# Performance work log

Measured on AMD Instinct MI355X. Metric: run time of the kernel, lower is better.

The kernel has to match this reference:

```python
import jax, jax.numpy as jnp
import numpy as np

B, S, O = 65536, 32, 16  # batch, state_dim, observation_dim


def setup_inputs() -> dict:
    key = jax.random.key(0)
    k1, k2, k3, k4 = jax.random.split(key, 4)
    observation = jax.random.normal(k1, (B, O), dtype=jnp.float32)
    # SPD observation noise covariance per batch element
    L = 0.1 * jax.random.normal(k2, (B, O, O), dtype=jnp.float32)
    observation_noise = jnp.einsum('bij,bkj->bik', L, L) + 1e-3 * jnp.eye(O, dtype=jnp.float32)
    observation_matrix = 0.001 * jax.random.normal(k3, (O, S), dtype=jnp.float32)
    observation_bias = 1e-6 * jax.random.normal(k4, (O,), dtype=jnp.float32)
    prior_mean = jnp.zeros((S,), dtype=jnp.float32)
    prior_precision = jnp.eye(S, dtype=jnp.float32)
    return {
        'observation': observation,
        'observation_noise': observation_noise,
        'observation_matrix': observation_matrix,
        'observation_bias': observation_bias,
        'prior_mean': prior_mean,
        'prior_precision': prior_precision,
    }


def reference(observation, observation_noise, observation_matrix, observation_bias,
              prior_mean, prior_precision):
    # observation: [B, O]; observation_noise: [B, O, O]
    noise_prec = jnp.linalg.inv(observation_noise)                      # [B, O, O]
    HtR = jnp.einsum('os,bop->bsp', observation_matrix, noise_prec)     # H^T R^{-1}: [B, S, O]
    innovation_cov = jnp.einsum('bso,ot->bst', HtR, observation_matrix) # [B, S, S]
    posterior_covariance = jnp.linalg.inv(prior_precision + innovation_cov)  # [B, S, S]
    residual = jnp.einsum('bso,bo->bs', HtR, observation - observation_bias)[..., None]  # [B, S, 1]
    prior_term = (prior_precision @ prior_mean)[:, None]                # [S, 1]
    posterior_mean = posterior_covariance @ (prior_term + residual)     # [B, S, 1]
    return posterior_mean, posterior_covariance
```

## Files before the change

### kernel.cpp

```cpp
#include <hip/hip_runtime.h>
#include <hip/hip_bf16.h>


typedef __attribute__((ext_vector_type(8))) short bf16x8;
typedef __attribute__((ext_vector_type(4))) float f32x4;

__device__ __forceinline__ unsigned bf16rne(float f) {
    unsigned x = __float_as_uint(f);
    return (x + 0x7FFFu + ((x >> 16) & 1u)) >> 16;
}
__device__ __forceinline__ unsigned pack2(float a, float b) {
    return bf16rne(a) | (bf16rne(b) << 16);
}

__global__ void lgs_setup(const float* __restrict__ H, const float* __restrict__ bias,
                          const float* __restrict__ mu0, const float* __restrict__ P,
                          float* __restrict__ ws)
{
    __shared__ float pinv[32][33];
    __shared__ float Gsh[16][33];
    const int l = threadIdx.x;

    float m[32];
#pragma unroll
    for (int i = 0; i < 32; ++i)
        m[i] = (l < 32) ? P[i * 32 + l] : ((i == (l - 32)) ? 1.0f : 0.0f);

#pragma unroll
    for (int k = 0; k < 32; ++k) {
        float bc[32];
#pragma unroll
        for (int i = 0; i < 32; ++i) bc[i] = __shfl(m[i], k, 64);
        float a = m[k] * (1.0f / bc[k]);
#pragma unroll
        for (int i = 0; i < 32; ++i)
            if (i != k) m[i] -= bc[i] * a;
        m[k] = a;
    }
    if (l >= 32) {
        const int c = l - 32;
#pragma unroll
        for (int i = 0; i < 32; ++i) pinv[c][i] = m[i];
    }
    asm volatile("" ::: "memory");

    for (int idx = l; idx < 512; idx += 64) {
        int o = idx >> 5, s = idx & 31;
        float acc = 0.f;
        for (int u = 0; u < 32; ++u) acc += H[o * 32 + u] * pinv[s][u];
        Gsh[o][s] = acc;
    }
    asm volatile("" ::: "memory");

    for (int idx = l; idx < 256; idx += 64) {
        int j = idx >> 4, i = idx & 15;
        float acc = 0.f;
        for (int s = 0; s < 32; ++s) acc += Gsh[i][s] * H[j * 32 + s];
        ws[idx] = acc;
    }
    unsigned* wsu = (unsigned*)ws;
    for (int idx = l; idx < 512; idx += 64) {
        int r = idx >> 8, rem = idx & 255;
        int ll = rem >> 2, j = rem & 3;
        int mm = 16 * r + (ll & 15);
        int kb = (((ll >> 4) * 8) + 2 * j) & 15;
        wsu[768 + idx] = pack2(-0.5f * Gsh[kb][mm], -0.5f * Gsh[kb + 1][mm]);
    }
    for (int idx = l; idx < 1024; idx += 64) {
        int tt = idx >> 8, rem = idx & 255;
        int ll = rem >> 2, j = rem & 3;
        int row = 16 * (tt >> 1) + ((ll >> 4) << 2) + j;
        int col = 16 * (tt & 1) + (ll & 15);
        ws[1280 + idx] = pinv[col][row];
    }
    for (int idx = l; idx < 512; idx += 64) {
        int c = idx >> 8, rem = idx & 255;
        int ll = rem >> 2, j2 = rem & 3;
        int col = 16 * c + (ll & 15);
        int k = (((ll >> 4) * 8) + 2 * j2) & 15;
        wsu[2304 + idx] = pack2(0.5f * Gsh[k][col], 0.5f * Gsh[k + 1][col]);
    }
    if (l < 16) {
        float acc = bias[l];
        for (int s = 0; s < 32; ++s) acc += H[l * 32 + s] * mu0[s];
        ws[2816 + l] = acc;
    }
    if (l < 32) ws[2832 + l] = mu0[l];
}

#define BCAST16(x, K) __int_as_float(__builtin_amdgcn_ds_swizzle(__float_as_int(x), (((K) << 5) | 0x10)))

template <int K>
__device__ __forceinline__ void gj16(int t, float (&m)[16], float (&v)[16])
{
    if (t == K) m[K] = 1.0f / m[K];
    float bc[16];
#pragma unroll
    for (int i = 0; i < 16; ++i) bc[i] = BCAST16(m[i], K);
    float pk = m[K] * bc[K];
#pragma unroll
    for (int i = 0; i < 16; ++i)
        if (i != K) m[i] -= bc[i] * pk;
    m[K] = pk;
    float a = v[K] * bc[K];
#pragma unroll
    for (int i = 0; i < 16; ++i)
        if (i != K) v[i] -= bc[i] * a;
    v[K] = a;
}

__global__ __launch_bounds__(512, 4) void lgs_main(
    const float* __restrict__ obs, const float* __restrict__ noise,
    const float* __restrict__ ws,
    float* __restrict__ out_mean, float* __restrict__ out_cov, int B)
{
    __shared__ float ld[8192];

    const int tid  = threadIdx.x;
    const int l    = tid & 63;
    const int t    = tid & 15;
    const int slot = tid >> 4;
    const int wv   = tid >> 6;
    const int b    = blockIdx.x * 32 + slot;
    const int bb   = (b < B) ? b : (B - 1);

    const float* __restrict__ Acm  = ws;
    const float* __restrict__ cvec = ws + 2816;
    const float* __restrict__ m0v  = ws + 2832;

    float m[16], v[16];

    const float4* Rr = (const float4*)(noise + (size_t)bb * 256 + t * 16);
    const float4* Ar = (const float4*)(Acm + t * 16);
#pragma unroll
    for (int i = 0; i < 4; ++i) {
        float4 r = Rr[i], a = Ar[i];
        m[4*i+0] = r.x + a.x; m[4*i+1] = r.y + a.y;
        m[4*i+2] = r.z + a.z; m[4*i+3] = r.w + a.w;
    }
#pragma unroll
    for (int i = 0; i < 16; ++i) v[i] = (i == t) ? 1.0f : 0.0f;

    gj16<0>(t, m, v);   gj16<1>(t, m, v);   gj16<2>(t, m, v);   gj16<3>(t, m, v);
    gj16<4>(t, m, v);   gj16<5>(t, m, v);   gj16<6>(t, m, v);   gj16<7>(t, m, v);
    gj16<8>(t, m, v);   gj16<9>(t, m, v);   gj16<10>(t, m, v);  gj16<11>(t, m, v);
    gj16<12>(t, m, v);  gj16<13>(t, m, v);  gj16<14>(t, m, v);  gj16<15>(t, m, v);

    {
        const int xw = t & 3;
        float* wb = &ld[slot * 256 + t * 16];
        *(float4*)&wb[(0 ^ xw) << 2] = make_float4(v[0],  v[1],  v[2],  v[3]);
        *(float4*)&wb[(1 ^ xw) << 2] = make_float4(v[4],  v[5],  v[6],  v[7]);
        *(float4*)&wb[(2 ^ xw) << 2] = make_float4(v[8],  v[9],  v[10], v[11]);
        *(float4*)&wb[(3 ^ xw) << 2] = make_float4(v[12], v[13], v[14], v[15]);
    }

    const uint4*  AF4 = (const uint4*)(ws + 768);
    const uint4*  BG4 = (const uint4*)(ws + 2304);
    const float4* PF4 = (const float4*)(ws + 1280);
    uint4 a0u = AF4[l], a1u = AF4[64 + l];
    uint4 g0u = BG4[l], g1u = BG4[64 + l];
    bf16x8 A0, A1, Bg0, Bg1;
    __builtin_memcpy(&A0,  &a0u, 16);
    __builtin_memcpy(&A1,  &a1u, 16);
    __builtin_memcpy(&Bg0, &g0u, 16);
    __builtin_memcpy(&Bg1, &g1u, 16);
    float4 pq;
    f32x4 pfr0, pfr1, pfr2, pfr3;
    pq = PF4[l];        pfr0[0]=pq.x; pfr0[1]=pq.y; pfr0[2]=pq.z; pfr0[3]=pq.w;
    pq = PF4[64 + l];   pfr1[0]=pq.x; pfr1[1]=pq.y; pfr1[2]=pq.z; pfr1[3]=pq.w;
    pq = PF4[128 + l];  pfr2[0]=pq.x; pfr2[1]=pq.y; pfr2[2]=pq.z; pfr2[3]=pq.w;
    pq = PF4[192 + l];  pfr3[0]=pq.x; pfr3[1]=pq.y; pfr3[2]=pq.z; pfr3[3]=pq.w;

    const int ch = l & 15;
    const int gp = l >> 4;
    const int gq = (gp & 1) * 2;
    const int xq = ch & 3;
    const int xt = (ch & 1) << 2;
    const float4 cv = ((const float4*)cvec)[gp];
    const float mu0a = m0v[ch], mu0b = m0v[16 + ch];
    const f32x4 zero = {0.f, 0.f, 0.f, 0.f};

#pragma unroll
    for (int h = 0; h < 4; ++h) {
        const int sh  = wv * 4 + h;
        const int bh  = blockIdx.x * 32 + sh;
        const int bhc = (bh < B) ? bh : (B - 1);

        const float* qb = &ld[sh * 256 + ch * 16];
        float4 qa = *(const float4*)&qb[((gq    ) ^ xq) << 2];
        float4 qc = *(const float4*)&qb[((gq + 1) ^ xq) << 2];
        unsigned qarr[4] = { pack2(qa.x, qa.y), pack2(qa.z, qa.w),
                             pack2(qc.x, qc.y), pack2(qc.z, qc.w) };
        bf16x8 Qa; __builtin_memcpy(&Qa, qarr, 16);
        f32x4 d0 = __builtin_amdgcn_mfma_f32_16x16x32_bf16(Qa, Bg0, zero, 0, 0, 0);
        f32x4 d1 = __builtin_amdgcn_mfma_f32_16x16x32_bf16(Qa, Bg1, zero, 0, 0, 0);

        float4 yv = *(const float4*)(obs + (size_t)bhc * 16 + gp * 4);
        float z0 = yv.x - cv.x, z1 = yv.y - cv.y, z2 = yv.z - cv.z, z3 = yv.w - cv.w;
        float p0 = d0[0]*z0 + d0[1]*z1 + d0[2]*z2 + d0[3]*z3;
        float p1 = d1[0]*z0 + d1[1]*z1 + d1[2]*z2 + d1[3]*z3;
        p0 += __int_as_float(__builtin_amdgcn_ds_swizzle(__float_as_int(p0), 0x401F));
        p1 += __int_as_float(__builtin_amdgcn_ds_swizzle(__float_as_int(p1), 0x401F));
        p0 += __shfl_xor(p0, 32, 64);
        p1 += __shfl_xor(p1, 32, 64);
        if (bh < B) {
            if (gp == 0) out_mean[(size_t)bh * 32 + ch]      = mu0a + p0;
            if (gp == 1) out_mean[(size_t)bh * 32 + 16 + ch] = mu0b + p1;
        }

        unsigned* tb = (unsigned*)&ld[sh * 256];
        const int g2 = gp * 2;
        *(uint2*)&tb[      ch * 8 + (g2 ^ xt)] =
            make_uint2(pack2(d0[0], d0[1]), pack2(d0[2], d0[3]));
        *(uint2*)&tb[128 + ch * 8 + (g2 ^ xt)] =
            make_uint2(pack2(d1[0], d1[1]), pack2(d1[2], d1[3]));

        const int kp = (gp & 1) * 4;
        uint4 bu0 = *(const uint4*)&tb[      ch * 8 + (kp ^ xt)];
        uint4 bu1 = *(const uint4*)&tb[128 + ch * 8 + (kp ^ xt)];
        bf16x8 Bf0, Bf1;
        __builtin_memcpy(&Bf0, &bu0, 16);
        __builtin_memcpy(&Bf1, &bu1, 16);
        f32x4 s00 = __builtin_amdgcn_mfma_f32_16x16x32_bf16(A0, Bf0, pfr0, 0, 0, 0);
        f32x4 s01 = __builtin_amdgcn_mfma_f32_16x16x32_bf16(A0, Bf1, pfr1, 0, 0, 0);
        f32x4 s10 = __builtin_amdgcn_mfma_f32_16x16x32_bf16(A1, Bf0, pfr2, 0, 0, 0);
        f32x4 s11 = __builtin_amdgcn_mfma_f32_16x16x32_bf16(A1, Bf1, pfr3, 0, 0, 0);

        if (bh < B) {
            float* Sb = out_cov + (size_t)bh * 1024 + (gp * 4) * 32 + ch;
#pragma unroll
            for (int j = 0; j < 4; ++j) {
                Sb[j * 32]       = s00[j];
                Sb[j * 32 + 16]  = s01[j];
                Sb[j * 32 + 512] = s10[j];
                Sb[j * 32 + 528] = s11[j];
            }
        }
    }
}

extern "C" void kernel_launch(void* const* d_in, const int* in_sizes, int n_in,
                              void* d_out, int out_size, void* d_ws, size_t ws_size,
                              hipStream_t stream)
{
    const float* obs   = (const float*)d_in[0];
    const float* noise = (const float*)d_in[1];
    const float* H     = (const float*)d_in[2];
    const float* bias  = (const float*)d_in[3];
    const float* mu0   = (const float*)d_in[4];
    const float* P     = (const float*)d_in[5];
    float* ws = (float*)d_ws;

    const int B = in_sizes[0] / 16;
    float* out_mean = (float*)d_out;
    float* out_cov  = out_mean + (size_t)B * 32;

    lgs_setup<<<1, 64, 0, stream>>>(H, bias, mu0, P, ws);
    lgs_main<<<(B + 31) / 32, 512, 0, stream>>>(obs, noise, ws, out_mean, out_cov, B);
}
```

Baseline: 110.1 us.

## Vectorize covariance stores via symmetric transpose and use hardware bf16 packing

Covariance output stores change from 16 scalar strided writes per lane to 4 float4 writes. The kernel writes the MFMA accumulator rows as columns, which relies on the posterior covariance being symmetric and swaps the s01/s10 block positions to match. Software bf16 rounding is replaced by the HIP float2-to-bfloat162 intrinsic, and the mean store is merged into one predicated store. The transposed layout holds only if the computed result is exactly symmetric, so small bf16 asymmetries would now be written transposed.

```diff
diff --git a/kernel.cpp b/kernel.cpp
--- a/kernel.cpp
+++ b/kernel.cpp
@@ -11,6 +11,11 @@
 }
 __device__ __forceinline__ unsigned pack2(float a, float b) {
     return bf16rne(a) | (bf16rne(b) << 16);
+}
+__device__ __forceinline__ unsigned packrn(float a, float b) {
+    __hip_bfloat162 h = __float22bfloat162_rn(make_float2(a, b));
+    unsigned u; __builtin_memcpy(&u, &h, 4);
+    return u;
 }
 
 __global__ void lgs_setup(const float* __restrict__ H, const float* __restrict__ bias,
@@ -178,7 +183,7 @@
     const int xq = ch & 3;
     const int xt = (ch & 1) << 2;
     const float4 cv = ((const float4*)cvec)[gp];
-    const float mu0a = m0v[ch], mu0b = m0v[16 + ch];
+    const float mu0l = m0v[l & 31];
     const f32x4 zero = {0.f, 0.f, 0.f, 0.f};
 
 #pragma unroll
@@ -190,8 +195,8 @@
         const float* qb = &ld[sh * 256 + ch * 16];
         float4 qa = *(const float4*)&qb[((gq    ) ^ xq) << 2];
         float4 qc = *(const float4*)&qb[((gq + 1) ^ xq) << 2];
-        unsigned qarr[4] = { pack2(qa.x, qa.y), pack2(qa.z, qa.w),
-                             pack2(qc.x, qc.y), pack2(qc.z, qc.w) };
+        unsigned qarr[4] = { packrn(qa.x, qa.y), packrn(qa.z, qa.w),
+                             packrn(qc.x, qc.y), packrn(qc.z, qc.w) };
         bf16x8 Qa; __builtin_memcpy(&Qa, qarr, 16);
         f32x4 d0 = __builtin_amdgcn_mfma_f32_16x16x32_bf16(Qa, Bg0, zero, 0, 0, 0);
         f32x4 d1 = __builtin_amdgcn_mfma_f32_16x16x32_bf16(Qa, Bg1, zero, 0, 0, 0);
@@ -204,17 +209,17 @@
         p1 += __int_as_float(__builtin_amdgcn_ds_swizzle(__float_as_int(p1), 0x401F));
         p0 += __shfl_xor(p0, 32, 64);
         p1 += __shfl_xor(p1, 32, 64);
-        if (bh < B) {
-            if (gp == 0) out_mean[(size_t)bh * 32 + ch]      = mu0a + p0;
-            if (gp == 1) out_mean[(size_t)bh * 32 + 16 + ch] = mu0b + p1;
+        if (bh < B && l < 32) {
+            float muv = mu0l + ((l < 16) ? p0 : p1);
+            out_mean[(size_t)bh * 32 + l] = muv;
         }
 
         unsigned* tb = (unsigned*)&ld[sh * 256];
         const int g2 = gp * 2;
         *(uint2*)&tb[      ch * 8 + (g2 ^ xt)] =
-            make_uint2(pack2(d0[0], d0[1]), pack2(d0[2], d0[3]));
+            make_uint2(packrn(d0[0], d0[1]), packrn(d0[2], d0[3]));
         *(uint2*)&tb[128 + ch * 8 + (g2 ^ xt)] =
-            make_uint2(pack2(d1[0], d1[1]), pack2(d1[2], d1[3]));
+            make_uint2(packrn(d1[0], d1[1]), packrn(d1[2], d1[3]));
 
         const int kp = (gp & 1) * 4;
         uint4 bu0 = *(const uint4*)&tb[      ch * 8 + (kp ^ xt)];
@@ -228,14 +233,16 @@
         f32x4 s11 = __builtin_amdgcn_mfma_f32_16x16x32_bf16(A1, Bf1, pfr3, 0, 0, 0);
 
         if (bh < B) {
-            float* Sb = out_cov + (size_t)bh * 1024 + (gp * 4) * 32 + ch;
-#pragma unroll
-            for (int j = 0; j < 4; ++j) {
-                Sb[j * 32]       = s00[j];
-                Sb[j * 32 + 16]  = s01[j];
-                Sb[j * 32 + 512] = s10[j];
-                Sb[j * 32 + 528] = s11[j];
-            }
+            float* Sb = out_cov + (size_t)bh * 1024;
+            const int cb = gp * 4;
+            *(float4*)&Sb[ch * 32 + cb] =
+                make_float4(s00[0], s00[1], s00[2], s00[3]);
+            *(float4*)&Sb[ch * 32 + 16 + cb] =
+                make_float4(s10[0], s10[1], s10[2], s10[3]);
+            *(float4*)&Sb[(16 + ch) * 32 + cb] =
+                make_float4(s01[0], s01[1], s01[2], s01[3]);
+            *(float4*)&Sb[(16 + ch) * 32 + 16 + cb] =
+                make_float4(s11[0], s11[1], s11[2], s11[3]);
         }
     }
 }
```

Result: slower. 118.6 us (+7.7%).

## Fuse setup kernel into main kernel, recomputing constant tables per block in LDS

Applied to the files above, without the earlier changes.

Removes the separate single-block setup launch and instead has every block invert the 32x32 prior precision, form the G/A/P tables and store them in shared memory before its own batch work. This eliminates a kernel launch and the serial dependency between the two launches. In exchange each of the 2048 blocks redundantly does the 32-step Gauss-Jordan on one wave plus small matmuls behind barriers, and uses extra LDS, which may reduce occupancy.

```diff
diff --git a/kernel.cpp b/kernel.cpp
--- a/kernel.cpp
+++ b/kernel.cpp
@@ -11,81 +11,6 @@
 }
 __device__ __forceinline__ unsigned pack2(float a, float b) {
     return bf16rne(a) | (bf16rne(b) << 16);
-}
-
-__global__ void lgs_setup(const float* __restrict__ H, const float* __restrict__ bias,
-                          const float* __restrict__ mu0, const float* __restrict__ P,
-                          float* __restrict__ ws)
-{
-    __shared__ float pinv[32][33];
-    __shared__ float Gsh[16][33];
-    const int l = threadIdx.x;
-
-    float m[32];
-#pragma unroll
-    for (int i = 0; i < 32; ++i)
-        m[i] = (l < 32) ? P[i * 32 + l] : ((i == (l - 32)) ? 1.0f : 0.0f);
-
-#pragma unroll
-    for (int k = 0; k < 32; ++k) {
-        float bc[32];
-#pragma unroll
-        for (int i = 0; i < 32; ++i) bc[i] = __shfl(m[i], k, 64);
-        float a = m[k] * (1.0f / bc[k]);
-#pragma unroll
-        for (int i = 0; i < 32; ++i)
-            if (i != k) m[i] -= bc[i] * a;
-        m[k] = a;
-    }
-    if (l >= 32) {
-        const int c = l - 32;
-#pragma unroll
-        for (int i = 0; i < 32; ++i) pinv[c][i] = m[i];
-    }
-    asm volatile("" ::: "memory");
-
-    for (int idx = l; idx < 512; idx += 64) {
-        int o = idx >> 5, s = idx & 31;
-        float acc = 0.f;
-        for (int u = 0; u < 32; ++u) acc += H[o * 32 + u] * pinv[s][u];
-        Gsh[o][s] = acc;
-    }
-    asm volatile("" ::: "memory");
-
-    for (int idx = l; idx < 256; idx += 64) {
-        int j = idx >> 4, i = idx & 15;
-        float acc = 0.f;
-        for (int s = 0; s < 32; ++s) acc += Gsh[i][s] * H[j * 32 + s];
-        ws[idx] = acc;
-    }
-    unsigned* wsu = (unsigned*)ws;
-    for (int idx = l; idx < 512; idx += 64) {
-        int r = idx >> 8, rem = idx & 255;
-        int ll = rem >> 2, j = rem & 3;
-        int mm = 16 * r + (ll & 15);
-        int kb = (((ll >> 4) * 8) + 2 * j) & 15;
-        wsu[768 + idx] = pack2(-0.5f * Gsh[kb][mm], -0.5f * Gsh[kb + 1][mm]);
-    }
-    for (int idx = l; idx < 1024; idx += 64) {
-        int tt = idx >> 8, rem = idx & 255;
-        int ll = rem >> 2, j = rem & 3;
-        int row = 16 * (tt >> 1) + ((ll >> 4) << 2) + j;
-        int col = 16 * (tt & 1) + (ll & 15);
-        ws[1280 + idx] = pinv[col][row];
-    }
-    for (int idx = l; idx < 512; idx += 64) {
-        int c = idx >> 8, rem = idx & 255;
-        int ll = rem >> 2, j2 = rem & 3;
-        int col = 16 * c + (ll & 15);
-        int k = (((ll >> 4) * 8) + 2 * j2) & 15;
-        wsu[2304 + idx] = pack2(0.5f * Gsh[k][col], 0.5f * Gsh[k + 1][col]);
-    }
-    if (l < 16) {
-        float acc = bias[l];
-        for (int s = 0; s < 32; ++s) acc += H[l * 32 + s] * mu0[s];
-        ws[2816 + l] = acc;
-    }
-    if (l < 32) ws[2832 + l] = mu0[l];
 }
 
 #define BCAST16(x, K) __int_as_float(__builtin_amdgcn_ds_swizzle(__float_as_int(x), (((K) << 5) | 0x10)))
@@ -109,12 +34,14 @@
     v[K] = a;
 }
 
-__global__ __launch_bounds__(512, 4) void lgs_main(
+__global__ __launch_bounds__(512, 4) void lgs_fused(
     const float* __restrict__ obs, const float* __restrict__ noise,
-    const float* __restrict__ ws,
+    const float* __restrict__ H, const float* __restrict__ bias,
+    const float* __restrict__ mu0, const float* __restrict__ P,
     float* __restrict__ out_mean, float* __restrict__ out_cov, int B)
 {
     __shared__ float ld[8192];
+    __shared__ float tbl[2368];
 
     const int tid  = threadIdx.x;
     const int l    = tid & 63;
@@ -124,9 +51,81 @@
     const int b    = blockIdx.x * 32 + slot;
     const int bb   = (b < B) ? b : (B - 1);
 
-    const float* __restrict__ Acm  = ws;
-    const float* __restrict__ cvec = ws + 2816;
-    const float* __restrict__ m0v  = ws + 2832;
+    float* pinv_s = ld;
+    float* Gsh_s  = ld + 1056;
+    if (wv == 0) {
+        float sm[32];
+#pragma unroll
+        for (int i = 0; i < 32; ++i)
+            sm[i] = (l < 32) ? P[i * 32 + l] : ((i == (l - 32)) ? 1.0f : 0.0f);
+#pragma unroll
+        for (int k = 0; k < 32; ++k) {
+            float bc[32];
+#pragma unroll
+            for (int i = 0; i < 32; ++i) bc[i] = __shfl(sm[i], k, 64);
+            float a = sm[k] * (1.0f / bc[k]);
+#pragma unroll
+            for (int i = 0; i < 32; ++i)
+                if (i != k) sm[i] -= bc[i] * a;
+            sm[k] = a;
+        }
+        if (l >= 32) {
+            const int c = l - 32;
+#pragma unroll
+            for (int i = 0; i < 32; ++i) pinv_s[c * 33 + i] = sm[i];
+        }
+    }
+    __syncthreads();
+
+    {
+        const int o = tid >> 5, s = tid & 31;
+        float acc = 0.f;
+        for (int u = 0; u < 32; ++u) acc += H[o * 32 + u] * pinv_s[s * 33 + u];
+        Gsh_s[o * 33 + s] = acc;
+    }
+    __syncthreads();
+
+    unsigned* tblu = (unsigned*)tbl;
+    for (int idx = tid; idx < 256; idx += 512) {
+        const int j = idx >> 4, i = idx & 15;
+        float acc = 0.f;
+        for (int s = 0; s < 32; ++s) acc += Gsh_s[i * 33 + s] * H[j * 32 + s];
+        tbl[idx] = acc;
+    }
+    for (int idx = tid; idx < 1024; idx += 512) {
+        const int tt = idx >> 8, rem = idx & 255;
+        const int ll = rem >> 2, j = rem & 3;
+        const int row = 16 * (tt >> 1) + ((ll >> 4) << 2) + j;
+        const int col = 16 * (tt & 1) + (ll & 15);
+        tbl[256 + idx] = pinv_s[col * 33 + row];
+    }
+    for (int idx = tid; idx < 512; idx += 512) {
+        const int r = idx >> 8, rem = idx & 255;
+        const int ll = rem >> 2, j = rem & 3;
+        const int mm = 16 * r + (ll & 15);
+        const int kb = (((ll >> 4) * 8) + 2 * j) & 15;
+        tblu[1280 + idx] = pack2(-0.5f * Gsh_s[kb * 33 + mm],
+                                 -0.5f * Gsh_s[(kb + 1) * 33 + mm]);
+    }
+    for (int idx = tid; idx < 512; idx += 512) {
+        const int c = idx >> 8, rem = idx & 255;
+        const int ll = rem >> 2, j2 = rem & 3;
+        const int col = 16 * c + (ll & 15);
+        const int k = (((ll >> 4) * 8) + 2 * j2) & 15;
+        tblu[1792 + idx] = pack2(0.5f * Gsh_s[k * 33 + col],
+                                 0.5f * Gsh_s[(k + 1) * 33 + col]);
+    }
+    if (tid < 16) {
+        float acc = bias[tid];
+        for (int s = 0; s < 32; ++s) acc += H[tid * 32 + s] * mu0[s];
+        tbl[2304 + tid] = acc;
+    }
+    if (tid < 32) tbl[2320 + tid] = mu0[tid];
+    __syncthreads();
+
+    const float* __restrict__ Acm  = tbl;
+    const float* __restrict__ cvec = tbl + 2304;
+    const float* __restrict__ m0v  = tbl + 2320;
 
     float m[16], v[16];
 
@@ -155,9 +154,9 @@
         *(float4*)&wb[(3 ^ xw) << 2] = make_float4(v[12], v[13], v[14], v[15]);
     }
 
-    const uint4*  AF4 = (const uint4*)(ws + 768);
-    const uint4*  BG4 = (const uint4*)(ws + 2304);
-    const float4* PF4 = (const float4*)(ws + 1280);
+    const uint4*  AF4 = (const uint4*)(tbl + 1280);
+    const uint4*  BG4 = (const uint4*)(tbl + 1792);
+    const float4* PF4 = (const float4*)(tbl + 256);
     uint4 a0u = AF4[l], a1u = AF4[64 + l];
     uint4 g0u = BG4[l], g1u = BG4[64 + l];
     bf16x8 A0, A1, Bg0, Bg1;
@@ -250,12 +249,11 @@
     const float* bias  = (const float*)d_in[3];
     const float* mu0   = (const float*)d_in[4];
     const float* P     = (const float*)d_in[5];
-    float* ws = (float*)d_ws;
 
     const int B = in_sizes[0] / 16;
     float* out_mean = (float*)d_out;
     float* out_cov  = out_mean + (size_t)B * 32;
 
-    lgs_setup<<<1, 64, 0, stream>>>(H, bias, mu0, P, ws);
-    lgs_main<<<(B + 31) / 32, 512, 0, stream>>>(obs, noise, ws, out_mean, out_cov, B);
-}
+    lgs_fused<<<(B + 31) / 32, 512, 0, stream>>>(obs, noise, H, bias, mu0, P,
+                                                 out_mean, out_cov, B);
+}
```

After: 126.8 us. 15.2% more time.
